# Kernel optimization log

Hardware: AMD Instinct MI355X
Metric: run time of the kernel (lower is better)

Reference implementation:

```python
import jax, jax.numpy as jnp
import numpy as np

B, S, D, H = 2, 2048, 768, 12
HD = D // H  # head dim = 64

def setup_inputs() -> dict:
    key = jax.random.key(0)
    ks = jax.random.split(key, 9)
    s = 1.0 / np.sqrt(D)
    return {
        "x": jax.random.normal(ks[0], (B, S, D), dtype=jnp.float32),
        "Wq": jax.random.uniform(ks[1], (D, D), jnp.float32, -s, s),
        "bq": jax.random.uniform(ks[2], (D,), jnp.float32, -s, s),
        "Wk": jax.random.uniform(ks[3], (D, D), jnp.float32, -s, s),
        "bk": jax.random.uniform(ks[4], (D,), jnp.float32, -s, s),
        "Wv": jax.random.uniform(ks[5], (D, D), jnp.float32, -s, s),
        "bv": jax.random.uniform(ks[6], (D,), jnp.float32, -s, s),
        "Wo": jax.random.uniform(ks[7], (D, D), jnp.float32, -s, s),
        "bo": jax.random.uniform(ks[8], (D,), jnp.float32, -s, s),
    }

def reference(x, Wq, bq, Wk, bk, Wv, bv, Wo, bo):
    b, s, _ = x.shape
    # linear projections, split into heads: [b, h, s, hd]
    def proj(W, bias):
        y = x @ W + bias
        return y.reshape(b, s, H, HD).transpose(0, 2, 1, 3)
    q = proj(Wq, bq)
    k = proj(Wk, bk)
    v = proj(Wv, bv)
    scale = 1.0 / np.sqrt(HD).astype(np.float32)
    scores = jnp.einsum('bhqd,bhkd->bhqk', q, k) * scale
    attn = jax.nn.softmax(scores, axis=-1)
    out = jnp.einsum('bhqk,bhkd->bhqd', attn, v)
    out = out.transpose(0, 2, 1, 3).reshape(b, s, D)
    return out @ Wo + bo
```

## Files before the change

### kernel.cpp

```cpp
#include <hip/hip_runtime.h>
#include <math.h>

#define NH 12
#define SEQ 2048
#define DM 768
#define HD 64
#define NB 2
#define MT (NB * SEQ)
#define QSCL 0.18033688011112042591999058512524f

typedef short bf16x8 __attribute__((ext_vector_type(8)));
typedef float f32x16 __attribute__((ext_vector_type(16)));
typedef unsigned u32x2 __attribute__((ext_vector_type(2)));

__device__ __forceinline__ unsigned short bf16_rne(float x) {
    unsigned u = __float_as_uint(x);
    u += 0x7fffu + ((u >> 16) & 1u);
    return (unsigned short)(u >> 16);
}
__device__ __forceinline__ float bf16_tof(short h) {
    return __uint_as_float(((unsigned)(unsigned short)h) << 16);
}
__device__ __forceinline__ unsigned cvtpk(float lo, float hi) {
    unsigned r;
    asm("v_cvt_pk_bf16_f32 %0, %1, %2" : "=v"(r) : "v"(lo), "v"(hi));
    return r;
}

__device__ __forceinline__ void gl_lds16(const void* g, void* s) {
    __builtin_amdgcn_global_load_lds(
        (const __attribute__((address_space(1))) unsigned int*)g,
        (__attribute__((address_space(3))) unsigned int*)s, 16, 0, 0);
}

__device__ __forceinline__ f32x16 mfma32(bf16x8 a, bf16x8 b, f32x16 c) {
    return __builtin_amdgcn_mfma_f32_32x32x16_bf16(a, b, c, 0, 0, 0);
}

__device__ __forceinline__ bf16x8 gfrag(const char* base, int row, int physblk) {
    return *(const bf16x8*)(base + row * 64 + physblk * 16);
}
__device__ __forceinline__ bf16x8 afrag(const short* base, int row, int blk) {
    return *(const bf16x8*)(base + row * 64 + ((blk ^ (row & 7)) << 3));
}

__global__ __launch_bounds__(256)
void conv_all(const float* __restrict__ x,
              const float* __restrict__ Wq, const float* __restrict__ Wk,
              const float* __restrict__ Wv, const float* __restrict__ Wo,
              short* __restrict__ xg, short* __restrict__ wqkv,
              short* __restrict__ wo)
{
    int b = blockIdx.x;
    if (b < 1536) {
        const int idx = b * 256 + threadIdx.x;
        const int m = idx / 96, bk = idx % 96;
        const float* src = x + (size_t)m * DM + bk * 8;
        float4 v0 = *(const float4*)src;
        float4 v1 = *(const float4*)(src + 4);
        const float vv[8] = {v0.x, v0.y, v0.z, v0.w, v1.x, v1.y, v1.z, v1.w};
        union { short s[8]; int4 q; } hh;
#pragma unroll
        for (int j = 0; j < 8; j++) hh.s[j] = (short)bf16_rne(vv[j]);
        const int pb = (bk & ~3) | ((bk & 3) ^ ((m >> 1) & 3));
        *(int4*)(xg + (size_t)m * DM + pb * 8) = hh.q;
    } else {
        b -= 1536;
        const int z = b / 288;
        const float* __restrict__ W = (z == 0) ? Wq : (z == 1) ? Wk : (z == 2) ? Wv : Wo;
        short* __restrict__ wdst = (z == 3) ? wo : (wqkv + (size_t)z * 589824);
        const int idx = (b % 288) * 256 + threadIdx.x;
        const int n = idx % 768, bk = idx / 768;
        union { short s[8]; int4 q; } hh;
#pragma unroll
        for (int j = 0; j < 8; j++) hh.s[j] = (short)bf16_rne(W[(size_t)(bk * 8 + j) * DM + n]);
        const int pb = (bk & ~3) | ((bk & 3) ^ ((n >> 1) & 3));
        *(int4*)(wdst + (size_t)n * DM + pb * 8) = hh.q;
    }
}

template<bool SWAP>
__device__ __forceinline__ void qkv_loop(const char* pA, const char* pB,
                                         char* As, char* Bs,
                                         int t, f32x16* acc)
{
    const int w = t >> 6, l = t & 63;
    const int q32 = l & 31, half = l >> 5;
    const int sel = (q32 >> 1) & 3;
    const int arow  = 32 * (w & 1) + q32;
    const int brow0 = 64 * (w >> 1) + q32;
    char* const dA = As + w * 1024;
    char* const dB = Bs + w * 1024;

    auto stage = [&](int ki, int buf) {
        const size_t cb = (size_t)ki * 64;
        gl_lds16(pA + cb, dA + buf * 4096);
        gl_lds16(pB + cb, dB + buf * 8192);
        gl_lds16(pB + 64 * 1536 + cb, dB + buf * 8192 + 4096);
    };

    stage(0, 0);
    __syncthreads();

    for (int ki = 0; ki < 24; ki++) {
        const int cur = ki & 1;
        if (ki < 23) stage(ki + 1, cur ^ 1);
        const char* sA = As + cur * 4096;
        const char* sB = Bs + cur * 8192;
#pragma unroll
        for (int s = 0; s < 2; s++) {
            const int blk = (s * 2 + half) ^ sel;
            bf16x8 a  = gfrag(sA, arow, blk);
            bf16x8 b0 = gfrag(sB, brow0, blk);
            bf16x8 b1 = gfrag(sB, brow0 + 32, blk);
            if (SWAP) {
                acc[0] = mfma32(b0, a, acc[0]);
                acc[1] = mfma32(b1, a, acc[1]);
            } else {
                acc[0] = mfma32(a, b0, acc[0]);
                acc[1] = mfma32(a, b1, acc[1]);
            }
        }
        __syncthreads();
    }
}

__global__ __launch_bounds__(256)
void gemm_qkv(const short* __restrict__ xg, const short* __restrict__ wqkv,
              const float* __restrict__ bq, const float* __restrict__ bkv,
              const float* __restrict__ bv,
              short* __restrict__ qg, short* __restrict__ kg, short* __restrict__ vg)
{
    const int z = blockIdx.z;
    const short* __restrict__ Bw = wqkv + (size_t)z * 589824;
    const float* __restrict__ bias = (z == 0) ? bq : (z == 1) ? bkv : bv;

    __shared__ char As[8192], Bs[16384];
    const int t = threadIdx.x, w = t >> 6, l = t & 63;
    const int m0 = blockIdx.y * 64, n0 = blockIdx.x * 128;
    const int q32 = l & 31, half = l >> 5;

    const char* pA = (const char*)xg + (size_t)(m0 + (t >> 2)) * 1536 + (t & 3) * 16;
    const char* pB = (const char*)Bw + (size_t)(n0 + (t >> 2)) * 1536 + (t & 3) * 16;

    f32x16 acc[2];
#pragma unroll
    for (int i = 0; i < 2; i++)
#pragma unroll
        for (int r = 0; r < 16; r++) acc[i][r] = 0.f;

    if (z == 2) {
        qkv_loop<false>(pA, pB, As, Bs, t, acc);
        const int nbase = n0 + 64 * (w >> 1);
        const int h = nbase >> 6;
        const int mbase = m0 + 32 * (w & 1) + 4 * half;
        const int bb = mbase >> 11;
#pragma unroll
        for (int nt = 0; nt < 2; nt++) {
            const int hd = 32 * nt + q32;
            const float bia = bias[nbase + hd];
            short* vrow = vg + ((size_t)(bb * NH + h) * HD + hd) * SEQ;
#pragma unroll
            for (int g = 0; g < 4; g++) {
                const int ss0 = (mbase & 2047) + 8 * g;
                union { unsigned short u[4]; uint2 q; } pk;
#pragma unroll
                for (int j = 0; j < 4; j++)
                    pk.u[j] = bf16_rne(acc[nt][4 * g + j] + bia);
                const int blk = ss0 >> 3;
                const int phys = (blk & ~7) | ((blk & 7) ^ (hd & 7));
                *(uint2*)(vrow + phys * 8 + (ss0 & 7)) = pk.q;
            }
        }
    } else {
        qkv_loop<true>(pA, pB, As, Bs, t, acc);
        short* dst = (z == 0) ? qg : kg;
        const float scl = (z == 0) ? QSCL : 1.0f;
        const int mcol = m0 + 32 * (w & 1) + q32;
        const int bb = mcol >> 11, ss = mcol & 2047;
        const int h = (n0 + 64 * (w >> 1)) >> 6;
        short* drow = dst + ((size_t)(bb * NH + h) * SEQ + ss) * HD;
#pragma unroll
        for (int nt = 0; nt < 2; nt++)
#pragma unroll
            for (int g = 0; g < 4; g++) {
                const int hd0 = 32 * nt + 8 * g + 4 * half;
                float4 b4 = *(const float4*)&bias[(h << 6) + hd0];
                const float bb4[4] = {b4.x, b4.y, b4.z, b4.w};
                union { unsigned short u[4]; uint2 q; } pk;
#pragma unroll
                for (int j = 0; j < 4; j++)
                    pk.u[j] = bf16_rne((acc[nt][4 * g + j] + bb4[j]) * scl);
                const int phys = (hd0 >> 3) ^ (ss & 7);
                *(uint2*)(drow + phys * 8 + (hd0 & 7)) = pk.q;
            }
    }
}

__global__ __launch_bounds__(256)
void attn_mfma(const short* __restrict__ qg, const short* __restrict__ kg,
               const short* __restrict__ vg,
               short* __restrict__ opart, float* __restrict__ lpart)
{
    __shared__ __align__(16) short lds[24576];
    short* const sl0 = lds + 8192;
    short* const sl1 = lds + 16384;
    short* const sl2 = lds;

    const int t = threadIdx.x, w = t >> 6, l = t & 63;
    const int f = (blockIdx.x & 7) * 96 + (blockIdx.x >> 3);
    const int q0 = (f & 15) * 128;
    const int bh = (f >> 4) % 24;
    const int ks = f / 384;
    const char* qp = (const char*)(qg + (size_t)bh * SEQ * HD);
    const char* kp = (const char*)(kg + (size_t)bh * SEQ * HD);
    const char* vp = (const char*)(vg + (size_t)bh * HD * SEQ);
    const int kbase = ks * 1024;

    auto slot = [&](int i) -> short* {
        const int md = i % 3;
        return md == 0 ? sl0 : md == 1 ? sl1 : sl2;
    };
    auto stage_kv = [&](int tile, short* dst) {
        const int kb0 = kbase + tile * 64;
#pragma unroll
        for (int i = 0; i < 2; i++) {
            gl_lds16(kp + (size_t)(kb0 + w * 16 + i * 8) * 128 + l * 16,
                     (char*)dst + (w * 16 + i * 8) * 128);
            gl_lds16(vp + (size_t)(w * 16 + i * 8 + (l >> 3)) * 4096 + kb0 * 2 + (l & 7) * 16,
                     (char*)(dst + 4096) + (w * 16 + i * 8) * 128);
        }
    };

#pragma unroll
    for (int i = 0; i < 4; i++)
        gl_lds16(qp + (size_t)(q0 + w * 32 + i * 8) * 128 + l * 16,
                 (char*)lds + (w * 32 + i * 8) * 128);
    stage_kv(0, sl0);
    stage_kv(1, sl1);

    asm volatile("s_waitcnt vmcnt(8)" ::: "memory");

    const int half = l >> 5;
    const int q = l & 31;
    bf16x8 qf[4];
#pragma unroll
    for (int s = 0; s < 4; s++)
        qf[s] = afrag(lds, w * 32 + q, half + s * 2);
    __syncthreads();

    f32x16 oacc[2], lacc;
#pragma unroll
    for (int nt = 0; nt < 2; nt++)
#pragma unroll
        for (int r = 0; r < 16; r++) oacc[nt][r] = 0.f;
#pragma unroll
    for (int r = 0; r < 16; r++) lacc[r] = 0.f;

    bf16x8 onesf;
#pragma unroll
    for (int j = 0; j < 8; j++) onesf[j] = (short)0x3F80;

    f32x16 sacc[2];
#pragma unroll
    for (int nt = 0; nt < 2; nt++)
#pragma unroll
        for (int r = 0; r < 16; r++) sacc[nt][r] = 0.f;
#pragma unroll
    for (int s = 0; s < 4; s++)
#pragma unroll
        for (int nt = 0; nt < 2; nt++)
            sacc[nt] = mfma32(afrag(sl0, nt * 32 + q, half + s * 2), qf[s], sacc[nt]);

    for (int kti = 0; kti < 16; kti++) {
#pragma unroll
        for (int nt = 0; nt < 2; nt++)
#pragma unroll
            for (int r = 0; r < 16; r++) sacc[nt][r] = exp2f(sacc[nt][r]);

        bf16x8 pfs[4];
#pragma unroll
        for (int s = 0; s < 4; s++) {
            const int nt = s >> 1;
            const int rb = (s & 1) * 8;
            const unsigned p0 = cvtpk(sacc[nt][rb + 0], sacc[nt][rb + 1]);
            const unsigned p1 = cvtpk(sacc[nt][rb + 2], sacc[nt][rb + 3]);
            const unsigned p2 = cvtpk(sacc[nt][rb + 4], sacc[nt][rb + 5]);
            const unsigned p3 = cvtpk(sacc[nt][rb + 6], sacc[nt][rb + 7]);
            const u32x2 w02 = __builtin_amdgcn_permlane32_swap(p0, p2, false, false);
            const u32x2 w13 = __builtin_amdgcn_permlane32_swap(p1, p3, false, false);
            union { unsigned u[4]; bf16x8 v; } pf;
            pf.u[0] = w02[0];
            pf.u[1] = w13[0];
            pf.u[2] = w02[1];
            pf.u[3] = w13[1];
            pfs[s] = pf.v;
        }

        if (kti < 14) stage_kv(kti + 2, slot(kti + 2));

        if (kti < 15) {
            const short* kc = slot(kti + 1);
#pragma unroll
            for (int nt = 0; nt < 2; nt++)
#pragma unroll
                for (int r = 0; r < 16; r++) sacc[nt][r] = 0.f;
#pragma unroll
            for (int s = 0; s < 4; s++)
#pragma unroll
                for (int nt = 0; nt < 2; nt++)
                    sacc[nt] = mfma32(afrag(kc, nt * 32 + q, half + s * 2), qf[s], sacc[nt]);
        }

        const short* vc = slot(kti) + 4096;
#pragma unroll
        for (int s = 0; s < 4; s++) {
            lacc = mfma32(pfs[s], onesf, lacc);
#pragma unroll
            for (int nt2 = 0; nt2 < 2; nt2++)
                oacc[nt2] = mfma32(pfs[s], afrag(vc, nt2 * 32 + q, half + s * 2), oacc[nt2]);
        }
        __syncthreads();
    }

    const size_t base = (size_t)(ks * 24 + bh) * SEQ;
#pragma unroll
    for (int r = 0; r < 16; r++) {
        const int row = q0 + w * 32 + (r & 3) + 8 * (r >> 2) + 4 * half;
#pragma unroll
        for (int nt = 0; nt < 2; nt++)
            opart[(base + row) * 64 + nt * 32 + q] = (short)bf16_rne(oacc[nt][r]);
        if (q == 0) lpart[base + row] = lacc[r];
    }
}

__global__ __launch_bounds__(256)
void gemm_out(const short* __restrict__ opart, const float* __restrict__ lpart,
              const short* __restrict__ wt3, const float* __restrict__ bias,
              float* __restrict__ out)
{
    __shared__ char As[8192], Bs[8192];
    const int t = threadIdx.x, w = t >> 6, l = t & 63;
    const int m0 = blockIdx.y * 64, n0 = blockIdx.x * 64;
    const int q32 = l & 31, half = l >> 5;
    const int sel = (q32 >> 1) & 3;

    const int r = t >> 2, c4 = t & 3;
    const int m = m0 + r;
    const int b = m >> 11, s = m & 2047;
    char* const dAw = As + r * 64 + (c4 ^ ((r >> 1) & 3)) * 16;

    const char* pB = (const char*)wt3 + (size_t)(n0 + (t >> 2)) * 1536 + (t & 3) * 16;
    char* const dB = Bs + w * 1024;

    const int arow = 32 * (w & 1) + q32;
    const int brow = 32 * (w >> 1) + q32;

    f32x16 acc;
#pragma unroll
    for (int rr = 0; rr < 16; rr++) acc[rr] = 0.f;

    union i4u { short sh[8]; int4 q; };
    i4u o0, o1;
    float inv;

    auto loadA = [&](int ki) {
        const int h = ki >> 1;
        const size_t lrow = (size_t)(b * NH + h) * SEQ + s;
        const size_t obase = lrow * 64 + (ki & 1) * 32 + c4 * 8;
        o0.q = *(const int4*)(opart + obase);
        o1.q = *(const int4*)(opart + obase + (size_t)24 * SEQ * 64);
        inv = 1.0f / (lpart[lrow] + lpart[lrow + (size_t)24 * SEQ]);
    };
    auto writeA = [&](int buf) {
        i4u oa;
#pragma unroll
        for (int j = 0; j < 8; j++)
            oa.sh[j] = (short)bf16_rne((bf16_tof(o0.sh[j]) + bf16_tof(o1.sh[j])) * inv);
        *(int4*)(dAw + buf * 4096) = oa.q;
    };
    auto stageB = [&](int ki, int buf) {
        gl_lds16(pB + (size_t)ki * 64, dB + buf * 4096);
    };

    loadA(0); writeA(0); stageB(0, 0);
    __syncthreads();

    for (int ki = 0; ki < 24; ki++) {
        const int cur = ki & 1;
        if (ki < 23) { stageB(ki + 1, cur ^ 1); loadA(ki + 1); }
        const char* sA = As + cur * 4096;
        const char* sB = Bs + cur * 4096;
#pragma unroll
        for (int ss = 0; ss < 2; ss++) {
            const int blk = (ss * 2 + half) ^ sel;
            acc = mfma32(gfrag(sB, brow, blk), gfrag(sA, arow, blk), acc);
        }
        if (ki < 23) writeA(cur ^ 1);
        __syncthreads();
    }

    const int mcol = m0 + 32 * (w & 1) + q32;
    const int nb0 = n0 + 32 * (w >> 1) + 4 * half;
#pragma unroll
    for (int g = 0; g < 4; g++) {
        const int ng = nb0 + 8 * g;
        float4 b4 = *(const float4*)&bias[ng];
        float4 o;
        o.x = acc[4 * g + 0] + b4.x;
        o.y = acc[4 * g + 1] + b4.y;
        o.z = acc[4 * g + 2] + b4.z;
        o.w = acc[4 * g + 3] + b4.w;
        *(float4*)&out[(size_t)mcol * DM + ng] = o;
    }
}

extern "C" void kernel_launch(void* const* d_in, const int* in_sizes, int n_in,
                              void* d_out, int out_size, void* d_ws, size_t ws_size,
                              hipStream_t stream)
{
    const float* x  = (const float*)d_in[0];
    const float* Wq = (const float*)d_in[1];
    const float* bq = (const float*)d_in[2];
    const float* Wk = (const float*)d_in[3];
    const float* bk = (const float*)d_in[4];
    const float* Wv = (const float*)d_in[5];
    const float* bv = (const float*)d_in[6];
    const float* Wo = (const float*)d_in[7];
    const float* bo = (const float*)d_in[8];
    float* out = (float*)d_out;

    const size_t BUF = (size_t)MT * DM;
    short* base  = (short*)d_ws;
    short* wo    = base;
    short* qg    = base + 589824;
    short* kg    = qg + BUF;
    short* vg    = kg + BUF;
    short* opart = vg + BUF;
    float* lpart = (float*)(opart + (size_t)2 * 24 * SEQ * HD);
    short* xg    = opart;
    short* wqkv  = xg + BUF;

    conv_all<<<2688, 256, 0, stream>>>(x, Wq, Wk, Wv, Wo, xg, wqkv, wo);
    gemm_qkv<<<dim3(6, 64, 3), 256, 0, stream>>>(xg, wqkv, bq, bk, bv, qg, kg, vg);
    attn_mfma<<<768, 256, 0, stream>>>(qg, kg, vg, opart, lpart);
    gemm_out<<<dim3(12, 64), 256, 0, stream>>>(opart, lpart, wo, bo, out);
}
```

Baseline: 196.3 us.

## Split attention partial reduction into separate kernel and raise MFMA wave priority

Moves the merge of the two key-split attention partials (sum, divide by softmax denominator, bf16 round) out of the output-projection GEMM into a standalone attn_reduce kernel. That kernel writes a pre-swizzled bf16 activation matrix into the qg buffer. gemm_out can then stage A with async global-to-LDS copies the same way it stages B. Separately, the attention kernel raises wave priority around its MFMA section with s_setprio. The trade is an extra kernel launch and an extra round trip of the activation through global memory, in exchange for a simpler, better-pipelined GEMM that no longer recomputes the reduction in each of its 12 column blocks.

```diff
diff --git a/kernel.cpp b/kernel.cpp
--- a/kernel.cpp
+++ b/kernel.cpp
@@ -299,6 +299,7 @@
 
         if (kti < 14) stage_kv(kti + 2, slot(kti + 2));
 
+        __builtin_amdgcn_s_setprio(1);
         if (kti < 15) {
             const short* kc = slot(kti + 1);
 #pragma unroll
@@ -320,6 +321,7 @@
             for (int nt2 = 0; nt2 < 2; nt2++)
                 oacc[nt2] = mfma32(pfs[s], afrag(vc, nt2 * 32 + q, half + s * 2), oacc[nt2]);
         }
+        __builtin_amdgcn_s_setprio(0);
         __syncthreads();
     }
 
@@ -335,9 +337,29 @@
 }
 
 __global__ __launch_bounds__(256)
-void gemm_out(const short* __restrict__ opart, const float* __restrict__ lpart,
-              const short* __restrict__ wt3, const float* __restrict__ bias,
-              float* __restrict__ out)
+void attn_reduce(const short* __restrict__ opart, const float* __restrict__ lpart,
+                 short* __restrict__ ag)
+{
+    const int idx = blockIdx.x * 256 + threadIdx.x;
+    const int cg = idx & 7, row = idx >> 3;
+    const int bh = row >> 11, s = row & 2047;
+    union { short s[8]; int4 q; } a, b, o;
+    a.q = *(const int4*)(opart + ((size_t)bh * SEQ + s) * 64 + cg * 8);
+    b.q = *(const int4*)(opart + ((size_t)(24 + bh) * SEQ + s) * 64 + cg * 8);
+    const float inv = 1.0f / (lpart[(size_t)bh * SEQ + s] + lpart[(size_t)(24 + bh) * SEQ + s]);
+#pragma unroll
+    for (int j = 0; j < 8; j++)
+        o.s[j] = (short)bf16_rne((bf16_tof(a.s[j]) + bf16_tof(b.s[j])) * inv);
+    const int bb = bh / NH, h = bh % NH;
+    const int m = bb * SEQ + s;
+    const int blk = h * 8 + cg;
+    const int phys = (blk & ~3) | ((blk & 3) ^ ((m >> 1) & 3));
+    *(int4*)(ag + (size_t)m * DM + phys * 8) = o.q;
+}
+
+__global__ __launch_bounds__(256)
+void gemm_out(const short* __restrict__ ag, const short* __restrict__ wt3,
+              const float* __restrict__ bias, float* __restrict__ out)
 {
     __shared__ char As[8192], Bs[8192];
     const int t = threadIdx.x, w = t >> 6, l = t & 63;
@@ -345,12 +367,9 @@
     const int q32 = l & 31, half = l >> 5;
     const int sel = (q32 >> 1) & 3;
 
-    const int r = t >> 2, c4 = t & 3;
-    const int m = m0 + r;
-    const int b = m >> 11, s = m & 2047;
-    char* const dAw = As + r * 64 + (c4 ^ ((r >> 1) & 3)) * 16;
-
+    const char* pA = (const char*)ag  + (size_t)(m0 + (t >> 2)) * 1536 + (t & 3) * 16;
     const char* pB = (const char*)wt3 + (size_t)(n0 + (t >> 2)) * 1536 + (t & 3) * 16;
+    char* const dA = As + w * 1024;
     char* const dB = Bs + w * 1024;
 
     const int arow = 32 * (w & 1) + q32;
@@ -358,45 +377,27 @@
 
     f32x16 acc;
 #pragma unroll
-    for (int rr = 0; rr < 16; rr++) acc[rr] = 0.f;
-
-    union i4u { short sh[8]; int4 q; };
-    i4u o0, o1;
-    float inv;
-
-    auto loadA = [&](int ki) {
-        const int h = ki >> 1;
-        const size_t lrow = (size_t)(b * NH + h) * SEQ + s;
-        const size_t obase = lrow * 64 + (ki & 1) * 32 + c4 * 8;
-        o0.q = *(const int4*)(opart + obase);
-        o1.q = *(const int4*)(opart + obase + (size_t)24 * SEQ * 64);
-        inv = 1.0f / (lpart[lrow] + lpart[lrow + (size_t)24 * SEQ]);
+    for (int r = 0; r < 16; r++) acc[r] = 0.f;
+
+    auto stage = [&](int ki, int buf) {
+        const size_t cb = (size_t)ki * 64;
+        gl_lds16(pA + cb, dA + buf * 4096);
+        gl_lds16(pB + cb, dB + buf * 4096);
     };
-    auto writeA = [&](int buf) {
-        i4u oa;
-#pragma unroll
-        for (int j = 0; j < 8; j++)
-            oa.sh[j] = (short)bf16_rne((bf16_tof(o0.sh[j]) + bf16_tof(o1.sh[j])) * inv);
-        *(int4*)(dAw + buf * 4096) = oa.q;
-    };
-    auto stageB = [&](int ki, int buf) {
-        gl_lds16(pB + (size_t)ki * 64, dB + buf * 4096);
-    };
-
-    loadA(0); writeA(0); stageB(0, 0);
+
+    stage(0, 0);
     __syncthreads();
 
     for (int ki = 0; ki < 24; ki++) {
         const int cur = ki & 1;
-        if (ki < 23) { stageB(ki + 1, cur ^ 1); loadA(ki + 1); }
+        if (ki < 23) stage(ki + 1, cur ^ 1);
         const char* sA = As + cur * 4096;
         const char* sB = Bs + cur * 4096;
 #pragma unroll
-        for (int ss = 0; ss < 2; ss++) {
-            const int blk = (ss * 2 + half) ^ sel;
+        for (int s = 0; s < 2; s++) {
+            const int blk = (s * 2 + half) ^ sel;
             acc = mfma32(gfrag(sB, brow, blk), gfrag(sA, arow, blk), acc);
         }
-        if (ki < 23) writeA(cur ^ 1);
         __syncthreads();
     }
 
@@ -440,9 +441,11 @@
     float* lpart = (float*)(opart + (size_t)2 * 24 * SEQ * HD);
     short* xg    = opart;
     short* wqkv  = xg + BUF;
+    short* ag    = qg;
 
     conv_all<<<2688, 256, 0, stream>>>(x, Wq, Wk, Wv, Wo, xg, wqkv, wo);
     gemm_qkv<<<dim3(6, 64, 3), 256, 0, stream>>>(xg, wqkv, bq, bk, bv, qg, kg, vg);
     attn_mfma<<<768, 256, 0, stream>>>(qg, kg, vg, opart, lpart);
-    gemm_out<<<dim3(12, 64), 256, 0, stream>>>(opart, lpart, wo, bo, out);
-}
+    attn_reduce<<<1536, 256, 0, stream>>>(opart, lpart, ag);
+    gemm_out<<<dim3(12, 64), 256, 0, stream>>>(ag, wo, bo, out);
+}
```

Measured after the change: 193.4 us. Within noise of the previous version (-1.5%).
